# Kernel tuning notes

Measured on AMD Instinct MI355X. Metric: run time of the kernel, lower is better.

## Reference

```python
import jax, jax.numpy as jnp
import numpy as np

BETA = 0.25      # commitment loss weight
DECAY = 0.99     # EMA decay
EPS = 1e-5       # Laplace smoothing for counts


def setup_inputs() -> dict:
    key = jax.random.key(0)
    k1, k2, k3 = jax.random.split(key, 3)
    B, d, h, w, K = 16, 64, 64, 64, 1024
    z_e = jax.random.normal(k1, (B, d, h, w), dtype=jnp.float32)
    codebook = jax.random.normal(k2, (K, d), dtype=jnp.float32)
    ema_count = jnp.ones((K,), dtype=jnp.float32)
    ema_sum = jax.random.normal(k3, (K, d), dtype=jnp.float32)
    return {"z_e": z_e, "codebook": codebook, "ema_count": ema_count, "ema_sum": ema_sum}


def reference(z_e, codebook, ema_count, ema_sum):
    B, d, h, w = z_e.shape
    K = codebook.shape[0]
    # [B,d,h,w] -> [N,d], N = B*h*w
    z_flat = jnp.transpose(z_e, (0, 2, 3, 1)).reshape(-1, d)
    # squared euclidean distances [N,K]
    dist = (jnp.sum(z_flat * z_flat, axis=1, keepdims=True)
            - 2.0 * (z_flat @ codebook.T)
            + jnp.sum(codebook * codebook, axis=1)[None, :])
    indices = jnp.argmin(dist, axis=1)                      # [N] int
    e_k = codebook[indices].reshape(B, h, w, d).transpose(0, 3, 1, 2)  # [B,d,h,w]

    # --- EMA codebook update (training mode, no grad) ---
    zf = jax.lax.stop_gradient(z_flat)
    counts = jax.ops.segment_sum(jnp.ones((zf.shape[0],), dtype=zf.dtype), indices, num_segments=K)
    sums = jax.ops.segment_sum(zf, indices, num_segments=K)
    new_count = ema_count * DECAY + (1.0 - DECAY) * counts
    new_sum = ema_sum * DECAY + (1.0 - DECAY) * sums
    n = jnp.sum(new_count)
    count_s = (new_count + EPS) / (n + K * EPS) * n
    new_codebook = new_sum / count_s[:, None]

    # straight-through estimator
    e_k_ste = z_e + jax.lax.stop_gradient(e_k - z_e)
    L_commit = (jnp.mean((z_e - jax.lax.stop_gradient(e_k)) ** 2)
                + BETA * jnp.mean((jax.lax.stop_gradient(z_e) - e_k) ** 2))
    return (e_k_ste, indices.reshape(B, h, w), L_commit, new_codebook, new_count, new_sum)
```

## Files before the change

kernel.cpp:

```cpp
#include <hip/hip_runtime.h>
#include <hip/hip_bf16.h>
#include <hip/hip_fp16.h>

#define NB 16
#define DD 64
#define HW 4096
#define NTOT 65536
#define KC 1024

#define O_EK   0
#define O_IDX  4194304
#define O_L    4259840
#define O_CB   4259841
#define O_CNT  4325377
#define O_SUM  4326401

#define WS_IDX    0
#define WS_LCPART 65536
#define WS_N      66048
#define WS_CNORM  66560
#define WS_PSUM   67584
#define WS_PCNT   329728
#define WS_CBH    399360
#define WS_CBL    432128

typedef _Float16 v8h __attribute__((ext_vector_type(8)));
typedef float    v4f __attribute__((ext_vector_type(4)));
typedef unsigned short ush;

__global__ __launch_bounds__(256) void k_pre(const float* __restrict__ cb,
                                             const float* __restrict__ ema_count,
                                             float* __restrict__ cnorm,
                                             float* __restrict__ n_ws,
                                             unsigned short* __restrict__ cbh,
                                             unsigned short* __restrict__ cbl) {
    const int t = threadIdx.x;
    const int w = (blockIdx.x * 256 + t) >> 6;
    const int l = t & 63;
    float s = 0.f;
    if (l < 16) {
        float4 v = *(const float4*)(cb + (size_t)w * DD + l * 4);
        s = v.x * v.x + v.y * v.y + v.z * v.z + v.w * v.w;
    }
#pragma unroll
    for (int m = 1; m <= 8; m <<= 1) s += __shfl_xor(s, m, 64);
    if (l == 0) cnorm[w] = s;

    const int e4 = blockIdx.x * 256 + t;
    if (e4 < 16384) {
        float4 v4 = ((const float4*)cb)[e4];
        float sx = -2.f * v4.x, sy = -2.f * v4.y, sz = -2.f * v4.z, sw = -2.f * v4.w;
        __half hx = __float2half(sx), hy = __float2half(sy),
               hz = __float2half(sz), hw2 = __float2half(sw);
        ushort4 h4 = { __half_as_ushort(hx), __half_as_ushort(hy),
                       __half_as_ushort(hz), __half_as_ushort(hw2) };
        ((ushort4*)cbh)[e4] = h4;
        ushort4 l4 = { __half_as_ushort(__float2half(sx - __half2float(hx))),
                       __half_as_ushort(__float2half(sy - __half2float(hy))),
                       __half_as_ushort(__float2half(sz - __half2float(hz))),
                       __half_as_ushort(__float2half(sw - __half2float(hw2))) };
        ((ushort4*)cbl)[e4] = l4;
    }

    if (blockIdx.x == 0) {
        __shared__ float red[256];
        red[t] = ema_count[t] + ema_count[t + 256] + ema_count[t + 512] + ema_count[t + 768];
        __syncthreads();
        for (int s2 = 128; s2 >= 1; s2 >>= 1) {
            if (t < s2) red[t] += red[t + s2];
            __syncthreads();
        }
        if (t == 0) n_ws[0] = 0.99f * red[0] + 0.01f * 65536.0f;
    }
}

__global__ __launch_bounds__(512) void k_argmin(const float* __restrict__ z_e,
                                                const float* __restrict__ cbf,
                                                const unsigned short* __restrict__ cbh,
                                                const unsigned short* __restrict__ cbl,
                                                const float* __restrict__ cnorm,
                                                unsigned short* __restrict__ idx16,
                                                float* __restrict__ out) {
    __shared__ __align__(16) unsigned char ldsAB[32768];
    __shared__ __align__(16) float slab[2048];
    __shared__ int idx_lds[128];
    __shared__ int flagrows[128];
    __shared__ int flagi1[128];
    __shared__ int flagi2[128];
    __shared__ int nflag;

    ush (*A2h)[128][8]  = (ush(*)[128][8])(ldsAB);
    ush (*A2l)[128][8]  = (ush(*)[128][8])(ldsAB + 16384);
    ush (*B2h)[8][64][8] = (ush(*)[8][64][8])(ldsAB);
    ush (*B2l)[8][64][8] = (ush(*)[8][64][8])(ldsAB + 16384);

    const int t  = threadIdx.x;
    const int n0 = blockIdx.x * 128;
    const int bb  = n0 >> 12;
    const int hw0 = n0 & 4095;
    const float* zbase = z_e + (size_t)bb * (DD * HW) + hw0;

    if (t == 0) nflag = 0;

    {
        const int jr   = t >> 5;
        const int m4   = (t & 31) << 2;
        const int chl  = t >> 8;
        const int cm   = t & 127;
        const int half = (t >> 7) & 1;
        for (int sl = 0; sl < 4; ++sl) {
            if (sl) __syncthreads();
            float4 v = *(const float4*)(zbase + (size_t)(sl * 16 + jr) * HW + m4);
            *(float4*)&slab[jr * 128 + m4] = v;
            __syncthreads();
            unsigned hv[2], lv[2];
#pragma unroll
            for (int p = 0; p < 2; ++p) {
                int jj = chl * 8 + half * 4 + p * 2;
                float v0 = slab[jj * 128 + cm];
                float v1 = slab[(jj + 1) * 128 + cm];
                __half h0 = __float2half(v0), h1 = __float2half(v1);
                __half l0 = __float2half(v0 - __half2float(h0));
                __half l1 = __float2half(v1 - __half2float(h1));
                hv[p] = (unsigned)__half_as_ushort(h0) | ((unsigned)__half_as_ushort(h1) << 16);
                lv[p] = (unsigned)__half_as_ushort(l0) | ((unsigned)__half_as_ushort(l1) << 16);
            }
            uint2 hq = {hv[0], hv[1]}, lq = {lv[0], lv[1]};
            *(uint2*)&A2h[sl * 2 + chl][cm][half * 4] = hq;
            *(uint2*)&A2l[sl * 2 + chl][cm][half * 4] = lq;
        }
    }
    __syncthreads();

    const int w    = t >> 6;
    const int lane = t & 63;
    const int c    = lane & 15;
    const int q    = lane >> 4;

    v8h Afh[2], Afl[2];
    {
        int m = 16 * w + c;
#pragma unroll
        for (int s = 0; s < 2; ++s) {
            Afh[s] = *(const v8h*)&A2h[s * 4 + q][m][0];
            Afl[s] = *(const v8h*)&A2l[s * 4 + q][m][0];
        }
    }
    __syncthreads();

    const int ch0   = t >> 6;
    const int code0 = t & 63;

    {
        size_t g0 = ((size_t)code0) * 64 + ch0 * 8;
        *(uint4*)&B2h[0][ch0][code0][0] = *(const uint4*)(cbh + g0);
        *(uint4*)&B2l[0][ch0][code0][0] = *(const uint4*)(cbl + g0);
    }
    __syncthreads();

    float m1f[4], m2f[4];
#pragma unroll
    for (int r = 0; r < 4; ++r) { m1f[r] = 3.4e38f; m2f[r] = 3.4e38f; }

    for (int kt = 0; kt < 16; ++kt) {
        const int cur = kt & 1, nxt = cur ^ 1;
        uint4 ph0, pl0;
        if (kt < 15) {
            size_t g0 = ((size_t)((kt + 1) * 64 + code0)) * 64 + ch0 * 8;
            ph0 = *(const uint4*)(cbh + g0);
            pl0 = *(const uint4*)(cbl + g0);
        }

#pragma unroll
        for (int sub = 0; sub < 4; ++sub) {
            const int cl = sub * 16 + c;
            v8h Bfh0 = *(const v8h*)&B2h[cur][q][cl][0];
            v8h Bfh1 = *(const v8h*)&B2h[cur][4 + q][cl][0];
            v8h Bfl0 = *(const v8h*)&B2l[cur][q][cl][0];
            v8h Bfl1 = *(const v8h*)&B2l[cur][4 + q][cl][0];
            const unsigned kg = (unsigned)(kt * 64 + cl);
            const float cnc = cnorm[kg];
            v4f acc = {cnc, cnc, cnc, cnc};
            acc = __builtin_amdgcn_mfma_f32_16x16x32_f16(Afh[0], Bfh0, acc, 0, 0, 0);
            acc = __builtin_amdgcn_mfma_f32_16x16x32_f16(Afh[1], Bfh1, acc, 0, 0, 0);
            acc = __builtin_amdgcn_mfma_f32_16x16x32_f16(Afh[0], Bfl0, acc, 0, 0, 0);
            acc = __builtin_amdgcn_mfma_f32_16x16x32_f16(Afh[1], Bfl1, acc, 0, 0, 0);
            acc = __builtin_amdgcn_mfma_f32_16x16x32_f16(Afl[0], Bfh0, acc, 0, 0, 0);
            acc = __builtin_amdgcn_mfma_f32_16x16x32_f16(Afl[1], Bfh1, acc, 0, 0, 0);
#pragma unroll
            for (int r = 0; r < 4; ++r) {
                unsigned vu = (__float_as_uint(acc[r]) & 0xFFFFFC00u) | kg;
                float vp = __uint_as_float(vu);
                m2f[r] = __builtin_amdgcn_fmed3f(m1f[r], m2f[r], vp);
                m1f[r] = fminf(m1f[r], vp);
            }
        }

        if (kt < 15) {
            *(uint4*)&B2h[nxt][ch0][code0][0] = ph0;
            *(uint4*)&B2l[nxt][ch0][code0][0] = pl0;
        }
        __syncthreads();
    }

#pragma unroll
    for (int r = 0; r < 4; ++r) {
        float a = m1f[r], b2 = m2f[r];
#pragma unroll
        for (int mask = 1; mask <= 8; mask <<= 1) {
            float o1 = __shfl_xor(a, mask, 64);
            float o2 = __shfl_xor(b2, mask, 64);
            float mx = fmaxf(a, o1);
            a  = fminf(a, o1);
            b2 = fminf(fminf(b2, o2), mx);
        }
        if (c == 0) {
            int row = 16 * w + q * 4 + r;
            int i1 = (int)(__float_as_uint(a) & 1023u);
            idx_lds[row] = i1;
            float margin = fmaf(fabsf(a), 6e-4f, 0.0015f);
            if (b2 - a < margin) {
                int p = atomicAdd(&nflag, 1);
                flagrows[p] = row;
                flagi1[p] = i1;
                flagi2[p] = (int)(__float_as_uint(b2) & 1023u);
            }
        }
    }
    __syncthreads();

    {
        int nf = nflag;
        for (int f = w; f < nf; f += 8) {
            int row = flagrows[f], i1 = flagi1[f], i2x = flagi2[f];
            const float* zrow = zbase + row;
            float zj = zrow[(size_t)lane * HW];
            float p1 = zj * cbf[(size_t)i1  * DD + lane];
            float p2 = zj * cbf[(size_t)i2x * DD + lane];
#pragma unroll
            for (int mask = 1; mask <= 32; mask <<= 1) {
                p1 += __shfl_xor(p1, mask, 64);
                p2 += __shfl_xor(p2, mask, 64);
            }
            if (lane == 0) {
                float d1 = fmaf(-2.0f, p1, cnorm[i1]);
                float d2 = fmaf(-2.0f, p2, cnorm[i2x]);
                if (d2 < d1 || (d2 == d1 && i2x < i1)) idx_lds[row] = i2x;
            }
        }
    }
    __syncthreads();

    if (t < 128) {
        int bi = idx_lds[t];
        out[O_IDX + n0 + t] = (float)bi;
        idx16[n0 + t] = (unsigned short)bi;
    }
}

__global__ __launch_bounds__(1024) void k_out(const unsigned short* __restrict__ idx16,
                                              const float* __restrict__ z_e,
                                              const float* __restrict__ cb,
                                              float* __restrict__ psum,
                                              int* __restrict__ pcnt,
                                              float* __restrict__ lc_part,
                                              float* __restrict__ out) {
    __shared__ float acc[KC];
    __shared__ int bins[KC];
    __shared__ float cbj[KC];
    __shared__ float lcr[16];
    const int j = blockIdx.x & 63;
    const int c = blockIdx.x >> 6;
    const int t = threadIdx.x;
    acc[t] = 0.f;
    bins[t] = 0;
    cbj[t] = cb[(size_t)t * DD + j];
    __syncthreads();
    const float* zj = z_e + (size_t)j * HW;
    float* oj = out + O_EK + (size_t)j * HW;
    const int base = c * 16384;
    float lc = 0.f;
#pragma unroll
    for (int i = 0; i < 4; ++i) {
        int n4 = base + i * 4096 + t * 4;
        int b = n4 >> 12, hw = n4 & 4095;
        size_t zoff = (size_t)b * (DD * HW) + hw;
        float4 z4 = *(const float4*)(zj + zoff);
        ushort4 k4 = *(const ushort4*)(idx16 + n4);
        float e0 = cbj[k4.x], e1 = cbj[k4.y], e2 = cbj[k4.z], e3 = cbj[k4.w];
        float4 o4 = { z4.x + (e0 - z4.x), z4.y + (e1 - z4.y),
                      z4.z + (e2 - z4.z), z4.w + (e3 - z4.w) };
        *(float4*)(oj + zoff) = o4;
        float d0 = z4.x - e0, d1 = z4.y - e1, d2 = z4.z - e2, d3 = z4.w - e3;
        lc = fmaf(d0, d0, lc); lc = fmaf(d1, d1, lc);
        lc = fmaf(d2, d2, lc); lc = fmaf(d3, d3, lc);
        atomicAdd(&acc[k4.x], z4.x);
        atomicAdd(&acc[k4.y], z4.y);
        atomicAdd(&acc[k4.z], z4.z);
        atomicAdd(&acc[k4.w], z4.w);
        if (j == 0) {
            atomicAdd(&bins[k4.x], 1); atomicAdd(&bins[k4.y], 1);
            atomicAdd(&bins[k4.z], 1); atomicAdd(&bins[k4.w], 1);
        }
    }
    __syncthreads();
    psum[(size_t)c * 65536 + j * 1024 + t] = acc[t];
    if (j == 0) pcnt[c * 1024 + t] = bins[t];
#pragma unroll
    for (int m = 32; m >= 1; m >>= 1) lc += __shfl_xor(lc, m, 64);
    if ((t & 63) == 0) lcr[t >> 6] = lc;
    __syncthreads();
    if (t == 0) {
        float s = 0.f;
#pragma unroll
        for (int u = 0; u < 16; ++u) s += lcr[u];
        lc_part[blockIdx.x] = s;
    }
}

__global__ __launch_bounds__(1024) void k_epi(const float* __restrict__ psum,
                                              const int* __restrict__ pcnt,
                                              const float* __restrict__ ema_sum,
                                              const float* __restrict__ ema_count,
                                              const float* __restrict__ n_ws,
                                              const float* __restrict__ lc_part,
                                              float* __restrict__ out) {
    const int t = threadIdx.x;
    const int e = blockIdx.x * 1024 + t;
    const int k = e >> 6, j = e & 63;
    float s4 = psum[j * 1024 + k] + psum[65536 + j * 1024 + k]
             + psum[131072 + j * 1024 + k] + psum[196608 + j * 1024 + k];
    float ns = ema_sum[e] * 0.99f + 0.01f * s4;
    out[O_SUM + e] = ns;
    int cnt = pcnt[k] + pcnt[1024 + k] + pcnt[2048 + k] + pcnt[3072 + k];
    float nc = ema_count[k] * 0.99f + 0.01f * (float)cnt;
    float n  = n_ws[0];
    float cs = (nc + 1e-5f) / (n + 1024.0f * 1e-5f) * n;
    out[O_CB + e] = ns / cs;
    if (blockIdx.x == 0) {
        int c2 = pcnt[t] + pcnt[1024 + t] + pcnt[2048 + t] + pcnt[3072 + t];
        out[O_CNT + t] = ema_count[t] * 0.99f + 0.01f * (float)c2;
    }
    if (blockIdx.x == 1) {
        __shared__ float red[512];
        if (t < 512) red[t] = (t < 256) ? lc_part[t] : 0.f;
        __syncthreads();
        for (int s = 256; s >= 1; s >>= 1) {
            if (t < s) red[t] += red[t + s];
            __syncthreads();
        }
        if (t == 0) out[O_L] = 1.25f * red[0] * (1.0f / 4194304.0f);
    }
}

extern "C" void kernel_launch(void* const* d_in, const int* in_sizes, int n_in,
                              void* d_out, int out_size, void* d_ws, size_t ws_size,
                              hipStream_t stream) {
    const float* z_e       = (const float*)d_in[0];
    const float* cb        = (const float*)d_in[1];
    const float* ema_count = (const float*)d_in[2];
    const float* ema_sum   = (const float*)d_in[3];
    float* out             = (float*)d_out;

    float* ws_f      = (float*)d_ws;
    unsigned short* idx16 = (unsigned short*)d_ws;
    float* lc_part   = ws_f + WS_LCPART;
    float* n_ws      = ws_f + WS_N;
    float* cnorm_ws  = ws_f + WS_CNORM;
    float* psum      = ws_f + WS_PSUM;
    int*   pcnt      = (int*)(ws_f + WS_PCNT);
    unsigned short* cbh = (unsigned short*)(ws_f + WS_CBH);
    unsigned short* cbl = (unsigned short*)(ws_f + WS_CBL);

    k_pre<<<256, 256, 0, stream>>>(cb, ema_count, cnorm_ws, n_ws, cbh, cbl);
    k_argmin<<<NTOT / 128, 512, 0, stream>>>(z_e, cb, cbh, cbl, cnorm_ws, idx16, out);
    k_out<<<256, 1024, 0, stream>>>(idx16, z_e, cb, psum, pcnt, lc_part, out);
    k_epi<<<64, 1024, 0, stream>>>(psum, pcnt, ema_sum, ema_count, n_ws, lc_part, out);
}
```

Measured before the change: 140.9 us.

## Restructure argmin tiling: waves split codes, each wave holds all 64 rows

The argmin kernel now processes 64 rows per block with 256 threads instead of 128 rows with 512 threads. Each wave keeps A fragments for all 64 rows in registers and handles a distinct 16-code slice of each 64-code tile, so every B fragment is loaded from LDS once per wave rather than four times. This cuts LDS traffic per MFMA and reuses B across row groups. The cost is more registers per thread (4x A fragments and min/second-min state), an extra cross-wave top-2 merge through LDS, and twice as many blocks each reloading the full codebook.

```diff
diff --git a/kernel.cpp b/kernel.cpp
--- a/kernel.cpp
+++ b/kernel.cpp
@@ -74,7 +74,7 @@
     }
 }
 
-__global__ __launch_bounds__(512) void k_argmin(const float* __restrict__ z_e,
+__global__ __launch_bounds__(256) void k_argmin(const float* __restrict__ z_e,
                                                 const float* __restrict__ cbf,
                                                 const unsigned short* __restrict__ cbh,
                                                 const unsigned short* __restrict__ cbl,
@@ -82,52 +82,55 @@
                                                 unsigned short* __restrict__ idx16,
                                                 float* __restrict__ out) {
     __shared__ __align__(16) unsigned char ldsAB[32768];
-    __shared__ __align__(16) float slab[2048];
-    __shared__ int idx_lds[128];
-    __shared__ int flagrows[128];
-    __shared__ int flagi1[128];
-    __shared__ int flagi2[128];
+    __shared__ float2 mm[4][64];
+    __shared__ int idx_lds[64];
+    __shared__ int flagrows[64];
+    __shared__ int flagi1[64];
+    __shared__ int flagi2[64];
     __shared__ int nflag;
 
-    ush (*A2h)[128][8]  = (ush(*)[128][8])(ldsAB);
-    ush (*A2l)[128][8]  = (ush(*)[128][8])(ldsAB + 16384);
+    ush (*A2h)[64][8] = (ush(*)[64][8])(ldsAB);
+    ush (*A2l)[64][8] = (ush(*)[64][8])(ldsAB + 8192);
+    float* slab = (float*)(ldsAB + 16384);
     ush (*B2h)[8][64][8] = (ush(*)[8][64][8])(ldsAB);
     ush (*B2l)[8][64][8] = (ush(*)[8][64][8])(ldsAB + 16384);
 
     const int t  = threadIdx.x;
-    const int n0 = blockIdx.x * 128;
+    const int n0 = blockIdx.x * 64;
     const int bb  = n0 >> 12;
     const int hw0 = n0 & 4095;
     const float* zbase = z_e + (size_t)bb * (DD * HW) + hw0;
 
     if (t == 0) nflag = 0;
 
+#pragma unroll
+    for (int p = 0; p < 4; ++p) {
+        int fidx = t + p * 256;
+        int j    = fidx >> 4;
+        int m4   = (fidx & 15) << 2;
+        *(float4*)&slab[j * 64 + m4] = *(const float4*)(zbase + (size_t)j * HW + m4);
+    }
+    __syncthreads();
     {
-        const int jr   = t >> 5;
-        const int m4   = (t & 31) << 2;
-        const int chl  = t >> 8;
-        const int cm   = t & 127;
-        const int half = (t >> 7) & 1;
-        for (int sl = 0; sl < 4; ++sl) {
-            if (sl) __syncthreads();
-            float4 v = *(const float4*)(zbase + (size_t)(sl * 16 + jr) * HW + m4);
-            *(float4*)&slab[jr * 128 + m4] = v;
-            __syncthreads();
-            unsigned hv[2], lv[2];
-#pragma unroll
-            for (int p = 0; p < 2; ++p) {
-                int jj = chl * 8 + half * 4 + p * 2;
-                float v0 = slab[jj * 128 + cm];
-                float v1 = slab[(jj + 1) * 128 + cm];
+        const int m = t & 63, qq = t >> 6;
+#pragma unroll
+        for (int cc = 0; cc < 2; ++cc) {
+            int ch = qq * 2 + cc;
+            unsigned hv[4], lv[4];
+#pragma unroll
+            for (int p = 0; p < 4; ++p) {
+                float v0 = slab[(ch * 8 + 2 * p) * 64 + m];
+                float v1 = slab[(ch * 8 + 2 * p + 1) * 64 + m];
                 __half h0 = __float2half(v0), h1 = __float2half(v1);
                 __half l0 = __float2half(v0 - __half2float(h0));
                 __half l1 = __float2half(v1 - __half2float(h1));
                 hv[p] = (unsigned)__half_as_ushort(h0) | ((unsigned)__half_as_ushort(h1) << 16);
                 lv[p] = (unsigned)__half_as_ushort(l0) | ((unsigned)__half_as_ushort(l1) << 16);
             }
-            uint2 hq = {hv[0], hv[1]}, lq = {lv[0], lv[1]};
-            *(uint2*)&A2h[sl * 2 + chl][cm][half * 4] = hq;
-            *(uint2*)&A2l[sl * 2 + chl][cm][half * 4] = lq;
+            uint4 hq = {hv[0], hv[1], hv[2], hv[3]};
+            uint4 lq = {lv[0], lv[1], lv[2], lv[3]};
+            *(uint4*)&A2h[ch][m][0] = hq;
+            *(uint4*)&A2l[ch][m][0] = lq;
         }
     }
     __syncthreads();
@@ -136,102 +139,131 @@
     const int lane = t & 63;
     const int c    = lane & 15;
     const int q    = lane >> 4;
-
-    v8h Afh[2], Afl[2];
-    {
-        int m = 16 * w + c;
+    const int wc   = w * 16 + c;
+
+    v8h Afh[4][2], Afl[4][2];
+#pragma unroll
+    for (int rg = 0; rg < 4; ++rg) {
+        int m = 16 * rg + c;
 #pragma unroll
         for (int s = 0; s < 2; ++s) {
-            Afh[s] = *(const v8h*)&A2h[s * 4 + q][m][0];
-            Afl[s] = *(const v8h*)&A2l[s * 4 + q][m][0];
-        }
-    }
-    __syncthreads();
-
-    const int ch0   = t >> 6;
-    const int code0 = t & 63;
-
-    {
-        size_t g0 = ((size_t)code0) * 64 + ch0 * 8;
-        *(uint4*)&B2h[0][ch0][code0][0] = *(const uint4*)(cbh + g0);
-        *(uint4*)&B2l[0][ch0][code0][0] = *(const uint4*)(cbl + g0);
-    }
-    __syncthreads();
-
-    float m1f[4], m2f[4];
-#pragma unroll
-    for (int r = 0; r < 4; ++r) { m1f[r] = 3.4e38f; m2f[r] = 3.4e38f; }
+            Afh[rg][s] = *(const v8h*)&A2h[s * 4 + q][m][0];
+            Afl[rg][s] = *(const v8h*)&A2l[s * 4 + q][m][0];
+        }
+    }
+    __syncthreads();
+
+    const int scode = t & 63;
+    const int sch   = t >> 6;
+
+#pragma unroll
+    for (int i = 0; i < 2; ++i) {
+        int ch = sch + 4 * i;
+        size_t g = ((size_t)scode) * 64 + ch * 8;
+        *(uint4*)&B2h[0][ch][scode][0] = *(const uint4*)(cbh + g);
+        *(uint4*)&B2l[0][ch][scode][0] = *(const uint4*)(cbl + g);
+    }
+    __syncthreads();
+
+    float m1f[4][4], m2f[4][4];
+#pragma unroll
+    for (int rg = 0; rg < 4; ++rg)
+#pragma unroll
+        for (int r = 0; r < 4; ++r) { m1f[rg][r] = 3.4e38f; m2f[rg][r] = 3.4e38f; }
 
     for (int kt = 0; kt < 16; ++kt) {
         const int cur = kt & 1, nxt = cur ^ 1;
-        uint4 ph0, pl0;
+        uint4 ph[2], pl[2];
         if (kt < 15) {
-            size_t g0 = ((size_t)((kt + 1) * 64 + code0)) * 64 + ch0 * 8;
-            ph0 = *(const uint4*)(cbh + g0);
-            pl0 = *(const uint4*)(cbl + g0);
-        }
-
-#pragma unroll
-        for (int sub = 0; sub < 4; ++sub) {
-            const int cl = sub * 16 + c;
-            v8h Bfh0 = *(const v8h*)&B2h[cur][q][cl][0];
-            v8h Bfh1 = *(const v8h*)&B2h[cur][4 + q][cl][0];
-            v8h Bfl0 = *(const v8h*)&B2l[cur][q][cl][0];
-            v8h Bfl1 = *(const v8h*)&B2l[cur][4 + q][cl][0];
-            const unsigned kg = (unsigned)(kt * 64 + cl);
-            const float cnc = cnorm[kg];
+#pragma unroll
+            for (int i = 0; i < 2; ++i) {
+                int ch = sch + 4 * i;
+                size_t g = ((size_t)((kt + 1) * 64 + scode)) * 64 + ch * 8;
+                ph[i] = *(const uint4*)(cbh + g);
+                pl[i] = *(const uint4*)(cbl + g);
+            }
+        }
+
+        v8h Bh0 = *(const v8h*)&B2h[cur][q][wc][0];
+        v8h Bh1 = *(const v8h*)&B2h[cur][4 + q][wc][0];
+        v8h Bl0 = *(const v8h*)&B2l[cur][q][wc][0];
+        v8h Bl1 = *(const v8h*)&B2l[cur][4 + q][wc][0];
+        const unsigned kg = (unsigned)(kt * 64 + wc);
+        const float cnc = cnorm[kg];
+
+#pragma unroll
+        for (int rg = 0; rg < 4; ++rg) {
             v4f acc = {cnc, cnc, cnc, cnc};
-            acc = __builtin_amdgcn_mfma_f32_16x16x32_f16(Afh[0], Bfh0, acc, 0, 0, 0);
-            acc = __builtin_amdgcn_mfma_f32_16x16x32_f16(Afh[1], Bfh1, acc, 0, 0, 0);
-            acc = __builtin_amdgcn_mfma_f32_16x16x32_f16(Afh[0], Bfl0, acc, 0, 0, 0);
-            acc = __builtin_amdgcn_mfma_f32_16x16x32_f16(Afh[1], Bfl1, acc, 0, 0, 0);
-            acc = __builtin_amdgcn_mfma_f32_16x16x32_f16(Afl[0], Bfh0, acc, 0, 0, 0);
-            acc = __builtin_amdgcn_mfma_f32_16x16x32_f16(Afl[1], Bfh1, acc, 0, 0, 0);
+            acc = __builtin_amdgcn_mfma_f32_16x16x32_f16(Afh[rg][0], Bh0, acc, 0, 0, 0);
+            acc = __builtin_amdgcn_mfma_f32_16x16x32_f16(Afh[rg][1], Bh1, acc, 0, 0, 0);
+            acc = __builtin_amdgcn_mfma_f32_16x16x32_f16(Afh[rg][0], Bl0, acc, 0, 0, 0);
+            acc = __builtin_amdgcn_mfma_f32_16x16x32_f16(Afh[rg][1], Bl1, acc, 0, 0, 0);
+            acc = __builtin_amdgcn_mfma_f32_16x16x32_f16(Afl[rg][0], Bh0, acc, 0, 0, 0);
+            acc = __builtin_amdgcn_mfma_f32_16x16x32_f16(Afl[rg][1], Bh1, acc, 0, 0, 0);
 #pragma unroll
             for (int r = 0; r < 4; ++r) {
                 unsigned vu = (__float_as_uint(acc[r]) & 0xFFFFFC00u) | kg;
                 float vp = __uint_as_float(vu);
-                m2f[r] = __builtin_amdgcn_fmed3f(m1f[r], m2f[r], vp);
-                m1f[r] = fminf(m1f[r], vp);
+                m2f[rg][r] = __builtin_amdgcn_fmed3f(m1f[rg][r], m2f[rg][r], vp);
+                m1f[rg][r] = fminf(m1f[rg][r], vp);
             }
         }
 
         if (kt < 15) {
-            *(uint4*)&B2h[nxt][ch0][code0][0] = ph0;
-            *(uint4*)&B2l[nxt][ch0][code0][0] = pl0;
+#pragma unroll
+            for (int i = 0; i < 2; ++i) {
+                int ch = sch + 4 * i;
+                *(uint4*)&B2h[nxt][ch][scode][0] = ph[i];
+                *(uint4*)&B2l[nxt][ch][scode][0] = pl[i];
+            }
         }
         __syncthreads();
     }
 
 #pragma unroll
-    for (int r = 0; r < 4; ++r) {
-        float a = m1f[r], b2 = m2f[r];
-#pragma unroll
-        for (int mask = 1; mask <= 8; mask <<= 1) {
-            float o1 = __shfl_xor(a, mask, 64);
-            float o2 = __shfl_xor(b2, mask, 64);
-            float mx = fmaxf(a, o1);
-            a  = fminf(a, o1);
-            b2 = fminf(fminf(b2, o2), mx);
-        }
-        if (c == 0) {
-            int row = 16 * w + q * 4 + r;
-            int i1 = (int)(__float_as_uint(a) & 1023u);
-            idx_lds[row] = i1;
-            float margin = fmaf(fabsf(a), 6e-4f, 0.0015f);
-            if (b2 - a < margin) {
-                int p = atomicAdd(&nflag, 1);
-                flagrows[p] = row;
-                flagi1[p] = i1;
-                flagi2[p] = (int)(__float_as_uint(b2) & 1023u);
-            }
+    for (int rg = 0; rg < 4; ++rg)
+#pragma unroll
+        for (int r = 0; r < 4; ++r) {
+            float a = m1f[rg][r], b2 = m2f[rg][r];
+#pragma unroll
+            for (int mask = 1; mask <= 8; mask <<= 1) {
+                float o1 = __shfl_xor(a, mask, 64);
+                float o2 = __shfl_xor(b2, mask, 64);
+                float mx = fmaxf(a, o1);
+                a  = fminf(a, o1);
+                b2 = fminf(fminf(b2, o2), mx);
+            }
+            if (c == 0) {
+                int row = 16 * rg + q * 4 + r;
+                mm[w][row] = make_float2(a, b2);
+            }
+        }
+    __syncthreads();
+
+    if (t < 64) {
+        float a = 3.4e38f, b2 = 3.4e38f;
+#pragma unroll
+        for (int ww = 0; ww < 4; ++ww) {
+            float2 v = mm[ww][t];
+            float mx = fmaxf(a, v.x);
+            a  = fminf(a, v.x);
+            b2 = fminf(fminf(b2, v.y), mx);
+        }
+        int i1 = (int)(__float_as_uint(a) & 1023u);
+        idx_lds[t] = i1;
+        float margin = fmaf(fabsf(a), 6e-4f, 0.0015f);
+        if (b2 - a < margin) {
+            int p = atomicAdd(&nflag, 1);
+            flagrows[p] = t;
+            flagi1[p] = i1;
+            flagi2[p] = (int)(__float_as_uint(b2) & 1023u);
         }
     }
     __syncthreads();
 
     {
         int nf = nflag;
-        for (int f = w; f < nf; f += 8) {
+        for (int f = w; f < nf; f += 4) {
             int row = flagrows[f], i1 = flagi1[f], i2x = flagi2[f];
             const float* zrow = zbase + row;
             float zj = zrow[(size_t)lane * HW];
@@ -251,7 +283,7 @@
     }
     __syncthreads();
 
-    if (t < 128) {
+    if (t < 64) {
         int bi = idx_lds[t];
         out[O_IDX + n0 + t] = (float)bi;
         idx16[n0 + t] = (unsigned short)bi;
@@ -373,7 +405,7 @@
     unsigned short* cbl = (unsigned short*)(ws_f + WS_CBL);
 
     k_pre<<<256, 256, 0, stream>>>(cb, ema_count, cnorm_ws, n_ws, cbh, cbl);
-    k_argmin<<<NTOT / 128, 512, 0, stream>>>(z_e, cb, cbh, cbl, cnorm_ws, idx16, out);
+    k_argmin<<<NTOT / 64, 256, 0, stream>>>(z_e, cb, cbh, cbl, cnorm_ws, idx16, out);
     k_out<<<256, 1024, 0, stream>>>(idx16, z_e, cb, psum, pcnt, lc_part, out);
     k_epi<<<64, 1024, 0, stream>>>(psum, pcnt, ema_sum, ema_count, n_ws, lc_part, out);
 }
```

New measurement: 166.7 us. 18.4% more time.
